# Performance work log

Measured on AMD Instinct MI355X. Metric: run time of the kernel, lower is better.

## Reference

```python
import jax, jax.numpy as jnp
import numpy as np

DIM = 256
NUM_HEADS = 8
RATIO = 4
K_SAMPLES = 2
B, C, H, W = 2, 256, 64, 64


def setup_inputs() -> dict:
    key = jax.random.key(0)
    ks = jax.random.split(key, 12)
    N_low = (H // RATIO) * (W // RATIO)
    s = 0.02
    return {
        "q_high_feat": jax.random.normal(ks[0], (B, C, H, W), dtype=jnp.float32),
        "k_high_feat": jax.random.normal(ks[1], (B, C, H, W), dtype=jnp.float32),
        "v_high_feat": jax.random.normal(ks[2], (B, C, H, W), dtype=jnp.float32),
        "coarse_attn_map": jax.random.uniform(ks[3], (B, N_low, N_low), dtype=jnp.float32),
        "Wq": jax.random.normal(ks[4], (C, C), dtype=jnp.float32) * s,
        "bq": jnp.zeros((C,), dtype=jnp.float32),
        "Wk": jax.random.normal(ks[5], (C, C), dtype=jnp.float32) * s,
        "bk": jnp.zeros((C,), dtype=jnp.float32),
        "Wv": jax.random.normal(ks[6], (C, C), dtype=jnp.float32) * s,
        "bv": jnp.zeros((C,), dtype=jnp.float32),
        "Wo": jax.random.normal(ks[7], (C, C), dtype=jnp.float32) * s,
        "bo": jnp.zeros((C,), dtype=jnp.float32),
    }


def _sparse_indices(coarse_attn_map, H, W):
    # top-k coarse blocks per low-res query, expanded to high-res key indices
    H_low, W_low = H // RATIO, W // RATIO
    Bm, N_low, _ = coarse_attn_map.shape
    _, topk = jax.lax.top_k(coarse_attn_map, K_SAMPLES)          # (B, N_low, k)
    r0 = (topk // W_low) * RATIO                                  # top-left row
    c0 = (topk % W_low) * RATIO                                   # top-left col
    dr, dc = jnp.meshgrid(jnp.arange(RATIO), jnp.arange(RATIO), indexing='ij')
    dr, dc = dr.reshape(-1), dc.reshape(-1)                       # (ratio^2,)
    rows = r0[..., None] + dr                                     # (B, N_low, k, r2)
    cols = c0[..., None] + dc
    idx1d = (rows * W + cols).reshape(Bm, N_low, -1)              # (B, N_low, k*r2)
    # each low-res query row is repeated ratio^2 times (as in the torch code)
    return jnp.repeat(idx1d, RATIO * RATIO, axis=1)               # (B, N_high, K)


def reference(q_high_feat, k_high_feat, v_high_feat, coarse_attn_map,
              Wq, bq, Wk, bk, Wv, bv, Wo, bo):
    Bm, Cm, Hm, Wm = q_high_feat.shape
    N = Hm * Wm
    hd = Cm // NUM_HEADS
    scale = hd ** -0.5

    q_seq = q_high_feat.reshape(Bm, Cm, N).transpose(0, 2, 1)     # (B, N, C)
    k_seq = k_high_feat.reshape(Bm, Cm, N).transpose(0, 2, 1)
    v_seq = v_high_feat.reshape(Bm, Cm, N).transpose(0, 2, 1)

    final_idx = _sparse_indices(coarse_attn_map, Hm, Wm)          # (B, N, K)
    K_len = final_idx.shape[-1]

    q_proj = q_seq @ Wq + bq
    k_proj = k_seq @ Wk + bk
    v_proj = v_seq @ Wv + bv

    gather = jax.vmap(lambda p, i: p[i])                          # per-batch gather
    k_sp = gather(k_proj, final_idx)                              # (B, N, K, C)
    v_sp = gather(v_proj, final_idx)

    q = q_proj.reshape(Bm, N, NUM_HEADS, hd).transpose(0, 2, 1, 3)            # (B,h,N,d)
    k = k_sp.reshape(Bm, N, K_len, NUM_HEADS, hd).transpose(0, 3, 1, 2, 4)    # (B,h,N,K,d)
    v = v_sp.reshape(Bm, N, K_len, NUM_HEADS, hd).transpose(0, 3, 1, 2, 4)

    attn = jnp.einsum('bhnd,bhnkd->bhnk', q, k) * scale
    attn = jax.nn.softmax(attn, axis=-1)
    x = jnp.einsum('bhnk,bhnkd->bhnd', attn, v)
    x = x.transpose(0, 2, 1, 3).reshape(Bm, N, Cm)
    out = x @ Wo + bo
    return out.transpose(0, 2, 1).reshape(Bm, Cm, Hm, Wm)
```

## Files before the change

### kernel.cpp

```cpp
#include <hip/hip_runtime.h>
#include <hip/hip_bf16.h>
#include <cstddef>

#define BB 2
#define CC 256
#define HH 64
#define WW 64
#define NN 4096
#define NH 8
#define HD 32
#define NLOW 256
#define KLEN 32

typedef __attribute__((ext_vector_type(8))) short short8;
typedef __attribute__((ext_vector_type(4))) float float4v;

__device__ __forceinline__ float b2f(short s) {
    union { unsigned u; float f; } x;
    x.u = ((unsigned)(unsigned short)s) << 16;
    return x.f;
}
__device__ __forceinline__ short f2b(float f) {
    __hip_bfloat16 h = __float2bfloat16(f);
    return __builtin_bit_cast(short, h);
}

__device__ __forceinline__ void async_copy16(const short* g, short* l) {
    __builtin_amdgcn_global_load_lds(
        (const __attribute__((address_space(1))) void*)g,
        (__attribute__((address_space(3))) void*)l, 16, 0, 0);
}

__device__ __forceinline__ void trans_tile(const float* __restrict__ src, size_t soff,
                                           int sld, short* __restrict__ dst,
                                           size_t doff, int dld) {
    __shared__ float tile[64 * 65];
    const int t = threadIdx.x;
    #pragma unroll
    for (int p = 0; p < 4; ++p) {
        int r  = p * 16 + (t >> 4);
        int c4 = (t & 15) * 4;
        float4v v = *(const float4v*)&src[soff + (size_t)r * sld + c4];
        tile[r * 65 + c4 + 0] = v[0];
        tile[r * 65 + c4 + 1] = v[1];
        tile[r * 65 + c4 + 2] = v[2];
        tile[r * 65 + c4 + 3] = v[3];
    }
    __syncthreads();
    #pragma unroll
    for (int p = 0; p < 2; ++p) {
        int n  = p * 32 + (t >> 3);
        int c0 = (t & 7) * 8;
        short8 o;
        #pragma unroll
        for (int j = 0; j < 8; ++j) o[j] = f2b(tile[(c0 + j) * 65 + n]);
        *(short8*)&dst[doff + (size_t)n * dld + c0] = o;
    }
}

__global__ __launch_bounds__(256) void prep_kernel(
    const float* __restrict__ q, const float* __restrict__ k,
    const float* __restrict__ v, const float* __restrict__ Wq,
    const float* __restrict__ Wk, const float* __restrict__ Wv,
    const float* __restrict__ Wo, const float* __restrict__ coarse,
    short* __restrict__ qt, short* __restrict__ kt, short* __restrict__ vt,
    short* __restrict__ Wt, int* __restrict__ fidx) {
    const int z = blockIdx.z;
    if (z < 6) {
        const float* src = (z < 2) ? q : (z < 4) ? k : v;
        short* dst       = (z < 2) ? qt : (z < 4) ? kt : vt;
        const int b = z & 1;
        const int n0 = blockIdx.x * 64, c0 = blockIdx.y * 64;
        trans_tile(src, (size_t)b * CC * NN + (size_t)c0 * NN + n0, NN,
                   dst, ((size_t)b * NN + n0) * CC + c0, CC);
        return;
    }
    const int id = blockIdx.y * 64 + blockIdx.x;
    if (id < 64) {
        const int wz = id >> 4, tile = id & 15;
        const float* src = (wz == 0) ? Wq : (wz == 1) ? Wk : (wz == 2) ? Wv : Wo;
        short* dst = Wt + (size_t)wz * CC * CC;
        const int co0 = (tile >> 2) * 64, ci0 = (tile & 3) * 64;
        trans_tile(src, (size_t)ci0 * CC + co0, CC,
                   dst, (size_t)co0 * CC + ci0, CC);
        return;
    }
    if (id >= 192) return;
    const int w = threadIdx.x >> 6, l = threadIdx.x & 63;
    const int row = (id - 64) * 4 + w;
    const float* r = coarse + (size_t)row * NLOW;
    float4v x = *(const float4v*)&r[l * 4];
    const int base = l * 4;
    float v1 = x[0]; int i1 = base;
    float v2 = x[1]; int i2 = base + 1;
    if (v2 > v1) { float tv = v1; v1 = v2; v2 = tv; int ti = i1; i1 = i2; i2 = ti; }
    #pragma unroll
    for (int j = 2; j < 4; ++j) {
        float e = x[j]; int ei = base + j;
        if (e > v1)      { v2 = v1; i2 = i1; v1 = e; i1 = ei; }
        else if (e > v2) { v2 = e;  i2 = ei; }
    }
    #pragma unroll
    for (int off = 1; off < 64; off <<= 1) {
        float ov1 = __shfl_xor(v1, off), ov2 = __shfl_xor(v2, off);
        int   oi1 = __shfl_xor(i1, off), oi2 = __shfl_xor(i2, off);
        bool aw = (v1 > ov1) || (v1 == ov1 && i1 < oi1);
        float nv1 = aw ? v1 : ov1;  int ni1 = aw ? i1 : oi1;
        float c1v = aw ? ov1 : v1;  int c1i = aw ? oi1 : i1;
        float c2v = aw ? v2 : ov2;  int c2i = aw ? i2 : oi2;
        bool bw = (c1v > c2v) || (c1v == c2v && c1i < c2i);
        v1 = nv1; i1 = ni1;
        v2 = bw ? c1v : c2v; i2 = bw ? c1i : c2i;
    }
    if (l < 32) {
        int s = l >> 4, jj = l & 15;
        int idx = s ? i2 : i1;
        int rr = jj >> 2, cc2 = jj & 3;
        fidx[(size_t)row * KLEN + l] =
            ((idx >> 4) * 4 + rr) * WW + (idx & 15) * 4 + cc2;
    }
}

template <int MT>
__device__ __forceinline__ void gemm_core(
    const short* __restrict__ A, int am0, const short* __restrict__ Bt, int bn0,
    short* As, short* Bs, float4v acc[MT][4]) {
    const int t = threadIdx.x;
    const int w = t >> 6, lane = t & 63;
    const int l16 = lane & 15, quad = lane >> 4;
    for (int k0 = 0; k0 < CC; k0 += 64) {
        __syncthreads();
        #pragma unroll
        for (int g = 0; g < 2 * MT; ++g) {
            int p = (w * 2 * MT + g) * 64 + lane;
            int m = p >> 3;
            int cl8 = (((p & 7) ^ (m & 7)) << 3);
            async_copy16(A + (size_t)(am0 + m) * CC + k0 + cl8,
                         As + (size_t)(w * 2 * MT + g) * 512);
        }
        #pragma unroll
        for (int g = 0; g < 2; ++g) {
            int p = (w * 2 + g) * 64 + lane;
            int m = p >> 3;
            int cl8 = (((p & 7) ^ (m & 7)) << 3);
            async_copy16(Bt + (size_t)(bn0 + m) * CC + k0 + cl8,
                         Bs + (size_t)(w * 2 + g) * 512);
        }
        __syncthreads();
        #pragma unroll
        for (int s = 0; s < 2; ++s) {
            short8 bf[4];
            #pragma unroll
            for (int nt = 0; nt < 4; ++nt) {
                const int Rb = nt * 16 + l16;
                bf[nt] = *(const short8*)((const char*)Bs + Rb * 128 +
                                          (((s * 4 + quad) ^ (Rb & 7)) << 4));
            }
            #pragma unroll
            for (int mt = 0; mt < MT; ++mt) {
                const int Ra = mt * 64 + 16 * w + l16;
                short8 af = *(const short8*)((const char*)As + Ra * 128 +
                                             (((s * 4 + quad) ^ (Ra & 7)) << 4));
                #pragma unroll
                for (int nt = 0; nt < 4; ++nt)
                    acc[mt][nt] = __builtin_amdgcn_mfma_f32_16x16x32_bf16(
                        af, bf[nt], acc[mt][nt], 0, 0, 0);
            }
        }
    }
}

__global__ __launch_bounds__(256) void proj_gemm(
    const short* __restrict__ qt, const short* __restrict__ kt,
    const short* __restrict__ vt, const short* __restrict__ Wt,
    const float* __restrict__ bq, const float* __restrict__ bk,
    const float* __restrict__ bv,
    short* __restrict__ qp, short* __restrict__ kp, short* __restrict__ vp) {
    const int which = blockIdx.z;
    const short* A  = which == 0 ? qt : which == 1 ? kt : vt;
    const short* B  = Wt + (size_t)which * CC * CC;
    const float* bias = which == 0 ? bq : which == 1 ? bk : bv;
    short* outp     = which == 0 ? qp : which == 1 ? kp : vp;
    const int am0 = blockIdx.x * 128;
    const int nt0 = blockIdx.y * 64;

    __shared__ short As[128 * 64];
    __shared__ short Bs[64 * 64];
    float4v acc[2][4];
    #pragma unroll
    for (int i = 0; i < 2; ++i)
        #pragma unroll
        for (int j = 0; j < 4; ++j) acc[i][j] = (float4v)(0.f);

    gemm_core<2>(A, am0, B, nt0, As, Bs, acc);

    const int t = threadIdx.x;
    const int w = t >> 6, lane = t & 63;
    const int l16 = lane & 15, quad = lane >> 4;
    #pragma unroll
    for (int mt = 0; mt < 2; ++mt)
        #pragma unroll
        for (int nt = 0; nt < 4; ++nt) {
            int col = nt0 + nt * 16 + l16;
            float bv_ = bias[col];
            #pragma unroll
            for (int r = 0; r < 4; ++r) {
                int m = am0 + mt * 64 + 16 * w + quad * 4 + r;
                outp[(size_t)m * CC + col] = f2b(acc[mt][nt][r] + bv_);
            }
        }
}

__global__ __launch_bounds__(256) void attn_out_kernel(
    const short* __restrict__ qp, const short* __restrict__ kp,
    const short* __restrict__ vp, const int* __restrict__ fidx,
    const short* __restrict__ Wto, const float* __restrict__ bo,
    float* __restrict__ out) {
    const int low = blockIdx.x, b = blockIdx.y;
    const int t = threadIdx.x;
    const int w = t >> 6, lane = t & 63;

    __shared__ short Ks[32 * 256];
    __shared__ short Vs[32 * 256];
    __shared__ short Xs[16 * 32 * 8];

    const int* frow = fidx + (size_t)(b * NLOW + low) * KLEN;
    #pragma unroll
    for (int c = 0; c < 4; ++c) {
        int key = w * 8 + c * 2 + (lane >> 5);
        int idx = frow[key];
        idx = idx < 0 ? 0 : (idx > NN - 1 ? NN - 1 : idx);
        const short* gk = kp + (size_t)(b * NN + idx) * CC + (lane & 31) * 8;
        const short* gv = vp + (size_t)(b * NN + idx) * CC + (lane & 31) * 8;
        async_copy16(gk, &Ks[(w * 8 + c * 2) * 256]);
        async_copy16(gv, &Vs[(w * 8 + c * 2) * 256]);
    }
    __syncthreads();

    const int qi = t >> 4, h = (t >> 1) & 7, dh = t & 1;
    const int n = low * 16 + qi;
    const short* qrow = qp + (size_t)(b * NN + n) * CC + h * HD + dh * 16;

    float qv[16];
    #pragma unroll
    for (int c = 0; c < 2; ++c) {
        short8 v = *(const short8*)&qrow[c * 8];
        #pragma unroll
        for (int e = 0; e < 8; ++e) qv[c * 8 + e] = b2f(v[e]);
    }

    const float scale = 0.17677669529663687f;
    float sc[KLEN];
    for (int j = 0; j < KLEN; ++j) {
        const short* kr = &Ks[j * 256 + h * HD + dh * 16];
        float s = 0.f;
        #pragma unroll
        for (int c = 0; c < 2; ++c) {
            short8 v = *(const short8*)&kr[c * 8];
            #pragma unroll
            for (int e = 0; e < 8; ++e) s += qv[c * 8 + e] * b2f(v[e]);
        }
        sc[j] = s;
    }
    float mx = -1e30f;
    #pragma unroll
    for (int j = 0; j < KLEN; ++j) {
        sc[j] = (sc[j] + __shfl_xor(sc[j], 1)) * scale;
        mx = fmaxf(mx, sc[j]);
    }
    float denom = 0.f;
    #pragma unroll
    for (int j = 0; j < KLEN; ++j) { sc[j] = __expf(sc[j] - mx); denom += sc[j]; }
    const float inv = 1.f / denom;

    float ov[16];
    #pragma unroll
    for (int d = 0; d < 16; ++d) ov[d] = 0.f;
    for (int j = 0; j < KLEN; ++j) {
        float p = sc[j] * inv;
        const short* vr = &Vs[j * 256 + h * HD + dh * 16];
        #pragma unroll
        for (int c = 0; c < 2; ++c) {
            short8 v = *(const short8*)&vr[c * 8];
            #pragma unroll
            for (int e = 0; e < 8; ++e) ov[c * 8 + e] += p * b2f(v[e]);
        }
    }

    #pragma unroll
    for (int c = 0; c < 2; ++c) {
        int lc = h * 4 + dh * 2 + c;
        int p = qi * 32 + (lc & ~7) + ((lc & 7) ^ (qi & 7));
        short8 v;
        #pragma unroll
        for (int e = 0; e < 8; ++e) v[e] = f2b(ov[c * 8 + e]);
        *(short8*)((char*)Xs + (size_t)p * 16) = v;
    }
    __syncthreads();

    const int l16 = lane & 15, quad = lane >> 4;
    float4v acc[4];
    #pragma unroll
    for (int i = 0; i < 4; ++i) acc[i] = (float4v)(0.f);

    #pragma unroll
    for (int s = 0; s < 8; ++s) {
        int lc = s * 4 + quad;
        int p = l16 * 32 + (lc & ~7) + ((lc & 7) ^ (l16 & 7));
        short8 af = *(const short8*)((const char*)Xs + (size_t)p * 16);
        #pragma unroll
        for (int nt = 0; nt < 4; ++nt) {
            int co = w * 64 + nt * 16 + l16;
            short8 bf = *(const short8*)(Wto + (size_t)co * CC + s * 32 + quad * 8);
            acc[nt] = __builtin_amdgcn_mfma_f32_16x16x32_bf16(af, bf, acc[nt], 0, 0, 0);
        }
    }

    const int nbase = low * 16 + quad * 4;
    #pragma unroll
    for (int nt = 0; nt < 4; ++nt) {
        int c = w * 64 + nt * 16 + l16;
        float bias = bo[c];
        float4v o;
        #pragma unroll
        for (int r = 0; r < 4; ++r) o[r] = acc[nt][r] + bias;
        *(float4v*)&out[(size_t)(b * CC + c) * NN + nbase] = o;
    }
}

extern "C" void kernel_launch(void* const* d_in, const int* in_sizes, int n_in,
                              void* d_out, int out_size, void* d_ws, size_t ws_size,
                              hipStream_t stream) {
    const float* q      = (const float*)d_in[0];
    const float* k      = (const float*)d_in[1];
    const float* v      = (const float*)d_in[2];
    const float* coarse = (const float*)d_in[3];
    const float* Wq     = (const float*)d_in[4];
    const float* bq     = (const float*)d_in[5];
    const float* Wk     = (const float*)d_in[6];
    const float* bk     = (const float*)d_in[7];
    const float* Wv     = (const float*)d_in[8];
    const float* bv     = (const float*)d_in[9];
    const float* Wo     = (const float*)d_in[10];
    const float* bo     = (const float*)d_in[11];

    char* ws = (char*)d_ws;
    const size_t MB4 = (size_t)BB * NN * CC * 2;
    short* qt = (short*)(ws);
    short* kt = (short*)(ws + MB4);
    short* vt = (short*)(ws + 2 * MB4);
    short* qp = (short*)(ws + 3 * MB4);
    short* kp = (short*)(ws + 4 * MB4);
    short* vp = (short*)(ws + 5 * MB4);
    short* Wt = (short*)(ws + 6 * MB4);
    int* fidx = (int*)(ws + 6 * MB4 + 4 * (size_t)CC * CC * 2);

    prep_kernel<<<dim3(64, 4, 7), 256, 0, stream>>>(q, k, v, Wq, Wk, Wv, Wo,
                                                    coarse, qt, kt, vt, Wt, fidx);
    proj_gemm<<<dim3(64, 4, 3), 256, 0, stream>>>(qt, kt, vt, Wt, bq, bk, bv,
                                                  qp, kp, vp);
    attn_out_kernel<<<dim3(NLOW, BB), 256, 0, stream>>>(qp, kp, vp, fidx,
                                                        Wt + 3 * CC * CC, bo,
                                                        (float*)d_out);
}
```

Baseline: 120.8 us.

## Fuse Q projection into attention kernel and use sync loads in GEMM

```diff
diff --git a/kernel.cpp b/kernel.cpp
--- a/kernel.cpp
+++ b/kernel.cpp
@@ -135,16 +135,16 @@
             int p = (w * 2 * MT + g) * 64 + lane;
             int m = p >> 3;
             int cl8 = (((p & 7) ^ (m & 7)) << 3);
-            async_copy16(A + (size_t)(am0 + m) * CC + k0 + cl8,
-                         As + (size_t)(w * 2 * MT + g) * 512);
+            *(short8*)((char*)As + (size_t)p * 16) =
+                *(const short8*)(A + (size_t)(am0 + m) * CC + k0 + cl8);
         }
         #pragma unroll
         for (int g = 0; g < 2; ++g) {
             int p = (w * 2 + g) * 64 + lane;
             int m = p >> 3;
             int cl8 = (((p & 7) ^ (m & 7)) << 3);
-            async_copy16(Bt + (size_t)(bn0 + m) * CC + k0 + cl8,
-                         Bs + (size_t)(w * 2 + g) * 512);
+            *(short8*)((char*)Bs + (size_t)p * 16) =
+                *(const short8*)(Bt + (size_t)(bn0 + m) * CC + k0 + cl8);
         }
         __syncthreads();
         #pragma unroll
@@ -171,16 +171,15 @@
 }
 
 __global__ __launch_bounds__(256) void proj_gemm(
-    const short* __restrict__ qt, const short* __restrict__ kt,
-    const short* __restrict__ vt, const short* __restrict__ Wt,
-    const float* __restrict__ bq, const float* __restrict__ bk,
-    const float* __restrict__ bv,
-    short* __restrict__ qp, short* __restrict__ kp, short* __restrict__ vp) {
+    const short* __restrict__ kt, const short* __restrict__ vt,
+    const short* __restrict__ Wt,
+    const float* __restrict__ bk, const float* __restrict__ bv,
+    short* __restrict__ kp, short* __restrict__ vp) {
     const int which = blockIdx.z;
-    const short* A  = which == 0 ? qt : which == 1 ? kt : vt;
-    const short* B  = Wt + (size_t)which * CC * CC;
-    const float* bias = which == 0 ? bq : which == 1 ? bk : bv;
-    short* outp     = which == 0 ? qp : which == 1 ? kp : vp;
+    const short* A  = which == 0 ? kt : vt;
+    const short* B  = Wt + (size_t)(which + 1) * CC * CC;
+    const float* bias = which == 0 ? bk : bv;
+    short* outp     = which == 0 ? kp : vp;
     const int am0 = blockIdx.x * 128;
     const int nt0 = blockIdx.y * 64;
 
@@ -212,18 +211,31 @@
 }
 
 __global__ __launch_bounds__(256) void attn_out_kernel(
-    const short* __restrict__ qp, const short* __restrict__ kp,
+    const short* __restrict__ qt, const short* __restrict__ kp,
     const short* __restrict__ vp, const int* __restrict__ fidx,
-    const short* __restrict__ Wto, const float* __restrict__ bo,
-    float* __restrict__ out) {
+    const short* __restrict__ Wt, const float* __restrict__ bq,
+    const float* __restrict__ bo, float* __restrict__ out) {
     const int low = blockIdx.x, b = blockIdx.y;
     const int t = threadIdx.x;
     const int w = t >> 6, lane = t & 63;
+    const int l16 = lane & 15, quad = lane >> 4;
 
     __shared__ short Ks[32 * 256];
     __shared__ short Vs[32 * 256];
-    __shared__ short Xs[16 * 32 * 8];
-
+    __shared__ short U[16 * 256];
+
+    const short* Wtq = Wt;
+    const short* Wto = Wt + (size_t)3 * CC * CC;
+
+    #pragma unroll
+    for (int g = 0; g < 2; ++g) {
+        int p = w * 128 + g * 64 + lane;
+        int m = p >> 5;
+        int pc = p & 31;
+        int lc = (pc & ~7) | ((pc & 7) ^ (m & 7));
+        async_copy16(qt + ((size_t)(b * NN + low * 16 + m) * CC + lc * 8),
+                     U + (size_t)(w * 128 + g * 64) * 8);
+    }
     const int* frow = fidx + (size_t)(b * NLOW + low) * KLEN;
     #pragma unroll
     for (int c = 0; c < 4; ++c) {
@@ -237,9 +249,34 @@
     }
     __syncthreads();
 
+    float4v qacc[4];
+    #pragma unroll
+    for (int i = 0; i < 4; ++i) qacc[i] = (float4v)(0.f);
+    #pragma unroll
+    for (int s = 0; s < 8; ++s) {
+        int lc = s * 4 + quad;
+        int p = l16 * 32 + (lc & ~7) + ((lc & 7) ^ (l16 & 7));
+        short8 af = *(const short8*)((const char*)U + (size_t)p * 16);
+        #pragma unroll
+        for (int nt = 0; nt < 4; ++nt) {
+            int co = w * 64 + nt * 16 + l16;
+            short8 bf = *(const short8*)(Wtq + (size_t)co * CC + s * 32 + quad * 8);
+            qacc[nt] = __builtin_amdgcn_mfma_f32_16x16x32_bf16(af, bf, qacc[nt], 0, 0, 0);
+        }
+    }
+    __syncthreads();
+    #pragma unroll
+    for (int nt = 0; nt < 4; ++nt) {
+        int co = w * 64 + nt * 16 + l16;
+        float bias = bq[co];
+        #pragma unroll
+        for (int r = 0; r < 4; ++r)
+            U[(size_t)(quad * 4 + r) * CC + co] = f2b(qacc[nt][r] + bias);
+    }
+    __syncthreads();
+
     const int qi = t >> 4, h = (t >> 1) & 7, dh = t & 1;
-    const int n = low * 16 + qi;
-    const short* qrow = qp + (size_t)(b * NN + n) * CC + h * HD + dh * 16;
+    const short* qrow = &U[(size_t)qi * CC + h * HD + dh * 16];
 
     float qv[16];
     #pragma unroll
@@ -286,6 +323,7 @@
             for (int e = 0; e < 8; ++e) ov[c * 8 + e] += p * b2f(v[e]);
         }
     }
+    __syncthreads();
 
     #pragma unroll
     for (int c = 0; c < 2; ++c) {
@@ -294,20 +332,18 @@
         short8 v;
         #pragma unroll
         for (int e = 0; e < 8; ++e) v[e] = f2b(ov[c * 8 + e]);
-        *(short8*)((char*)Xs + (size_t)p * 16) = v;
-    }
-    __syncthreads();
-
-    const int l16 = lane & 15, quad = lane >> 4;
+        *(short8*)((char*)U + (size_t)p * 16) = v;
+    }
+    __syncthreads();
+
     float4v acc[4];
     #pragma unroll
     for (int i = 0; i < 4; ++i) acc[i] = (float4v)(0.f);
-
     #pragma unroll
     for (int s = 0; s < 8; ++s) {
         int lc = s * 4 + quad;
         int p = l16 * 32 + (lc & ~7) + ((lc & 7) ^ (l16 & 7));
-        short8 af = *(const short8*)((const char*)Xs + (size_t)p * 16);
+        short8 af = *(const short8*)((const char*)U + (size_t)p * 16);
         #pragma unroll
         for (int nt = 0; nt < 4; ++nt) {
             int co = w * 64 + nt * 16 + l16;
@@ -349,17 +385,14 @@
     short* qt = (short*)(ws);
     short* kt = (short*)(ws + MB4);
     short* vt = (short*)(ws + 2 * MB4);
-    short* qp = (short*)(ws + 3 * MB4);
-    short* kp = (short*)(ws + 4 * MB4);
-    short* vp = (short*)(ws + 5 * MB4);
-    short* Wt = (short*)(ws + 6 * MB4);
-    int* fidx = (int*)(ws + 6 * MB4 + 4 * (size_t)CC * CC * 2);
+    short* kp = (short*)(ws + 3 * MB4);
+    short* vp = (short*)(ws + 4 * MB4);
+    short* Wt = (short*)(ws + 5 * MB4);
+    int* fidx = (int*)(ws + 5 * MB4 + 4 * (size_t)CC * CC * 2);
 
     prep_kernel<<<dim3(64, 4, 7), 256, 0, stream>>>(q, k, v, Wq, Wk, Wv, Wo,
                                                     coarse, qt, kt, vt, Wt, fidx);
-    proj_gemm<<<dim3(64, 4, 3), 256, 0, stream>>>(qt, kt, vt, Wt, bq, bk, bv,
-                                                  qp, kp, vp);
-    attn_out_kernel<<<dim3(NLOW, BB), 256, 0, stream>>>(qp, kp, vp, fidx,
-                                                        Wt + 3 * CC * CC, bo,
-                                                        (float*)d_out);
-}
+    proj_gemm<<<dim3(64, 4, 2), 256, 0, stream>>>(kt, vt, Wt, bk, bv, kp, vp);
+    attn_out_kernel<<<dim3(NLOW, BB), 256, 0, stream>>>(qt, kp, vp, fidx, Wt,
+                                                        bq, bo, (float*)d_out);
+}
```

Measured after the change: 124.8 us. 3.3% more time.
